# Optimization experiments

Measured on AMD Instinct MI355X. Metric: run time of the kernel, lower is better.

The kernel has to match this reference:

```python
import jax, jax.numpy as jnp
import numpy as np

N_EMBD = 2048
N_HEAD = 16
HEAD_DIM = N_EMBD // N_HEAD
LORA_R = 8
LORA_ALPHA = 1.0
LORA_SCALING = LORA_ALPHA / LORA_R


def setup_inputs() -> dict:
    key = jax.random.key(0)
    ks = jax.random.split(key, 10)
    B, T = 4, 2048
    init = LORA_ALPHA / LORA_R
    return {
        "x": jax.random.normal(ks[0], (B, T, N_EMBD), dtype=jnp.float32),
        "W_attn": jax.random.normal(ks[1], (N_EMBD, 3 * N_EMBD), dtype=jnp.float32) * 0.02,
        "b_attn": jnp.zeros((3 * N_EMBD,), dtype=jnp.float32),
        "lora_A_q": jax.random.normal(ks[2], (N_EMBD, LORA_R), dtype=jnp.float32) * init,
        "lora_B_q": jax.random.normal(ks[3], (LORA_R, N_EMBD), dtype=jnp.float32) * init,
        "lora_A_k": jax.random.normal(ks[4], (N_EMBD, LORA_R), dtype=jnp.float32) * init,
        "lora_B_k": jax.random.normal(ks[5], (LORA_R, N_EMBD), dtype=jnp.float32) * init,
        "W_proj": jax.random.normal(ks[6], (N_EMBD, N_EMBD), dtype=jnp.float32) * 0.02,
        "b_proj": jnp.zeros((N_EMBD,), dtype=jnp.float32),
    }


def _rotate_half(x):
    # torch: x1 = x[..., ::2]; x2 = x[..., 1::2]; cat((-x2, x1), -1)
    x1 = x[..., ::2]
    x2 = x[..., 1::2]
    return jnp.concatenate([-x2, x1], axis=-1)


def _rope_cos_sin(T, dtype):
    inv_freq = 1.0 / (10000.0 ** (jnp.arange(0, HEAD_DIM, 2, dtype=jnp.float32) / HEAD_DIM))
    t = jnp.arange(T, dtype=jnp.float32)
    freqs = jnp.einsum("i,j->ij", t, inv_freq)            # [T, D/2]
    emb = jnp.concatenate([freqs, freqs], axis=-1)          # [T, D]
    return jnp.cos(emb).astype(dtype), jnp.sin(emb).astype(dtype)


def reference(x, W_attn, b_attn, lora_A_q, lora_B_q, lora_A_k, lora_B_k, W_proj, b_proj):
    B, T, C = x.shape
    qkv = x @ W_attn + b_attn                                # [B,T,3C]
    q, k, v = jnp.split(qkv, 3, axis=2)
    # LoRA additions on q, k (applied to attn outputs, per module)
    q = q + (q @ lora_A_q) @ lora_B_q * LORA_SCALING
    k = k + (k @ lora_A_k) @ lora_B_k * LORA_SCALING

    def to_heads(z):
        return z.reshape(B, T, N_HEAD, HEAD_DIM).transpose(0, 2, 1, 3)  # [B,H,T,D]

    q, k, v = to_heads(q), to_heads(k), to_heads(v)
    cos, sin = _rope_cos_sin(T, x.dtype)                     # [T,D] each
    q = q * cos + _rotate_half(q) * sin
    k = k * cos + _rotate_half(k) * sin

    scale = 1.0 / jnp.sqrt(jnp.asarray(HEAD_DIM, dtype=x.dtype))
    scores = jnp.einsum("bhqd,bhkd->bhqk", q, k) * scale     # [B,H,T,T]
    causal = jnp.tril(jnp.ones((T, T), dtype=bool))
    scores = jnp.where(causal, scores, jnp.finfo(x.dtype).min)
    attn = jax.nn.softmax(scores, axis=-1)
    y = jnp.einsum("bhqk,bhkd->bhqd", attn, v)               # [B,H,T,D]
    y = y.transpose(0, 2, 1, 3).reshape(B, T, C)
    return y @ W_proj + b_proj
```

## Files before the change

kernel.cpp:

```cpp
#include <hip/hip_runtime.h>
#include <hip/hip_bf16.h>
#include <stdint.h>


typedef __attribute__((ext_vector_type(8))) short short8;
typedef __attribute__((ext_vector_type(4))) short short4v;
typedef __attribute__((ext_vector_type(4))) float floatx4;

#define EXP2F(x) __builtin_amdgcn_exp2f(x)

__device__ __forceinline__ float bf2f(short h) {
  union { unsigned int u; float f; } v;
  v.u = ((unsigned int)(unsigned short)h) << 16;
  return v.f;
}
__device__ __forceinline__ short f2bf(float f) {
  unsigned int u = __float_as_uint(f);
  unsigned int r = (u + 0x7FFFu + ((u >> 16) & 1u)) >> 16;
  return (short)r;
}
__device__ __forceinline__ short f2bf_n(float f) {
  __hip_bfloat16 h = __float2bfloat16(f);
  union { __hip_bfloat16 b; short s; } v; v.b = h; return v.s;
}

__device__ __forceinline__ void gload_lds16(const short* g, short* l) {
  __builtin_amdgcn_global_load_lds(
      (const __attribute__((address_space(1))) unsigned int*)g,
      (__attribute__((address_space(3))) unsigned int*)l, 16, 0, 0);
}

__device__ __forceinline__ void store_out(float* p, float v) { *p = v; }
__device__ __forceinline__ void store_out(short* p, float v) { *p = f2bf(v); }

__device__ __forceinline__ int xcd_swz(int orig, int nwg) {
  int q = nwg >> 3;
  return (orig & 7) * q + (orig >> 3);
}

#define SWZ(off, row) ((off) ^ (((row) & 7) << 3))

__global__ void k_f2b(const float* __restrict__ in, short* __restrict__ out, int n8) {
  int i = blockIdx.x * 256 + threadIdx.x;
  if (i >= n8) return;
  const float4* p = (const float4*)in + (size_t)i * 2;
  float4 a = p[0], b = p[1];
  short8 v;
  v[0] = f2bf(a.x); v[1] = f2bf(a.y); v[2] = f2bf(a.z); v[3] = f2bf(a.w);
  v[4] = f2bf(b.x); v[5] = f2bf(b.y); v[6] = f2bf(b.z); v[7] = f2bf(b.w);
  *(short8*)(out + (size_t)i * 8) = v;
}

__global__ void k_wT(const float* __restrict__ W, short* __restrict__ WT, int K, int N) {
  __shared__ float tile[32][33];
  int n0 = blockIdx.x * 32, k0 = blockIdx.y * 32;
  int tx = threadIdx.x, ty = threadIdx.y;
  #pragma unroll
  for (int i = 0; i < 4; i++)
    tile[ty + i * 8][tx] = W[(size_t)(k0 + ty + i * 8) * N + n0 + tx];
  __syncthreads();
  #pragma unroll
  for (int i = 0; i < 4; i++)
    WT[(size_t)(n0 + ty + i * 8) * K + k0 + tx] = f2bf(tile[tx][ty + i * 8]);
}

__global__ void k_ropetab(float* __restrict__ ct, float* __restrict__ st) {
  int t = blockIdx.x, j = threadIdx.x;
  float invf = powf(10000.0f, -(float)(2 * j) / 128.0f);
  float ang = (float)t * invf;
  ct[t * 64 + j] = cosf(ang);
  st[t * 64 + j] = sinf(ang);
}


#define GBAR __builtin_amdgcn_s_barrier();

#define RDA(QR) \
    _Pragma("unroll") for (int m_ = 0; m_ < 4; m_++) \
    _Pragma("unroll") for (int kk_ = 0; kk_ < 2; kk_++) { \
      int sA_ = ((QR) * 2 + wm) * 8192 + (m_ * 16 + c16) * 128 + kk_ * 64 + g * 16; \
      afr[m_][kk_] = *(const short8*)(Ab + ((sA_ ^ swzk) >> 1)); \
    }

#define RDBX(BB, QC, DST) \
    _Pragma("unroll") for (int n_ = 0; n_ < 2; n_++) \
    _Pragma("unroll") for (int kk_ = 0; kk_ < 2; kk_++) { \
      int sB_ = ((QC) * 4 + wn) * 4096 + (n_ * 16 + c16) * 128 + kk_ * 64 + g * 16; \
      DST[n_][kk_] = *(const short8*)((BB) + ((sB_ ^ swzk) >> 1)); \
    }

#define MM(QR, QC, BF) \
    __builtin_amdgcn_s_barrier(); \
    __builtin_amdgcn_s_setprio(1); \
    _Pragma("unroll") for (int kk_ = 0; kk_ < 2; kk_++) \
    _Pragma("unroll") for (int m_ = 0; m_ < 4; m_++) \
    _Pragma("unroll") for (int n_ = 0; n_ < 2; n_++) \
      acc[(QR) * 4 + m_][(QC) * 2 + n_] = __builtin_amdgcn_mfma_f32_16x16x32_bf16( \
          afr[m_][kk_], BF[n_][kk_], acc[(QR) * 4 + m_][(QC) * 2 + n_], 0, 0, 0); \
    __builtin_amdgcn_s_setprio(0);

template <typename OutT>
__global__ __launch_bounds__(512, 2) void k_gemm8(
    const short* __restrict__ A, const short* __restrict__ BT,
    const float* __restrict__ bias, OutT* __restrict__ C,
    int M, int N, int K)
{
  __shared__ __attribute__((aligned(16))) short lds[65536];
  const int tid = threadIdx.x;
  const int w = tid >> 6, l = tid & 63;
  const int g = l >> 4, c16 = l & 15;
  const int wm = w >> 2, wn = w & 3;
  const int swzk = (c16 & 7) << 4;

  const int nwg = gridDim.x * gridDim.y;
  const int wg = xcd_swz(blockIdx.y * gridDim.x + blockIdx.x, nwg);
  const int bm = wg % gridDim.x, bn = wg / gridDim.x;

  const short* Ablk = A + (size_t)bm * 256 * K;
  const short* Bblk = BT + (size_t)bn * 256 * K;

  floatx4 acc[8][4];
  #pragma unroll
  for (int i = 0; i < 8; i++)
    #pragma unroll
    for (int j = 0; j < 4; j++)
      acc[i][j] = (floatx4){0.f, 0.f, 0.f, 0.f};

  const int NT = K >> 6;
  const int L = NT >> 1;

  auto stageA = [&](int b, int h, int t) {
    short* dst = lds + b * 32768;
    int k0 = t * 64;
    #pragma unroll
    for (int j = 0; j < 2; j++) {
      int P = h * 2 + j;
      int sL = P * 8192 + tid * 16;
      int q = sL ^ (((sL >> 7) & 7) << 4);
      int row = (((((P & 1) << 1) | (P >> 1))) << 6) + ((sL >> 7) & 63);
      gload_lds16(Ablk + (size_t)row * K + k0 + ((q & 127) >> 1), dst + (sL >> 1));
    }
  };
  auto stageB = [&](int b, int h, int t) {
    short* dst = lds + b * 32768 + 16384;
    int k0 = t * 64;
    #pragma unroll
    for (int j = 0; j < 2; j++) {
      int sL = (h * 4 + 2 * j) * 4096 + tid * 16;
      int pos = sL >> 12;
      int q = sL ^ (((sL >> 7) & 7) << 4);
      int row = (((pos & 3) * 2 + (pos >> 2)) << 5) + ((sL >> 7) & 31);
      gload_lds16(Bblk + (size_t)row * K + k0 + ((q & 127) >> 1), dst + (sL >> 1));
    }
  };

  stageA(0, 0, 0); stageB(0, 0, 0); stageA(0, 1, 0); stageB(0, 1, 0);
  stageA(1, 0, 1); stageB(1, 0, 1); stageA(1, 1, 1); stageB(1, 1, 1);
  asm volatile("s_waitcnt vmcnt(8)" ::: "memory");
  __builtin_amdgcn_s_barrier();

  short8 bfr0[2][2], bfr1[2][2];
  RDBX(lds + 16384, 0, bfr0)

  #pragma unroll 1
  for (int i = 0; i < L; i++) {
    const int t2 = 2 * i + 2, t3 = 2 * i + 3;
    short8 afr[4][2];

    {
      const short* Ab = lds;
      RDA(0) if (i > 0) stageA(1, 1, 2 * i + 1);
      MM(0, 0, bfr0) GBAR
      RDBX(lds + 16384, 1, bfr1) if (t2 < NT) stageA(0, 0, t2);
      MM(0, 1, bfr1) GBAR
      RDA(1) if (t2 < NT) stageB(0, 0, t2);
      MM(1, 0, bfr0)
      if (t2 < NT) { asm volatile("s_waitcnt vmcnt(4)" ::: "memory"); }
      else         { asm volatile("s_waitcnt vmcnt(0)" ::: "memory"); }
      GBAR
      RDBX(lds + 49152, 0, bfr0) if (t2 < NT) stageB(0, 1, t2);
      MM(1, 1, bfr1) GBAR
    }
    {
      const short* Ab = lds + 32768;
      RDA(0) if (t2 < NT) stageA(0, 1, t2);
      MM(0, 0, bfr0) GBAR
      RDBX(lds + 49152, 1, bfr1) if (t3 < NT) stageA(1, 0, t3);
      MM(0, 1, bfr1) GBAR
      RDA(1) if (t3 < NT) stageB(1, 0, t3);
      MM(1, 0, bfr0)
      if (t3 < NT) { asm volatile("s_waitcnt vmcnt(4)" ::: "memory"); }
      else         { asm volatile("s_waitcnt vmcnt(0)" ::: "memory"); }
      GBAR
      if (t2 < NT) { RDBX(lds + 16384, 0, bfr0) }
      if (t3 < NT) stageB(1, 1, t3);
      MM(1, 1, bfr1) GBAR
    }
  }

  #pragma unroll
  for (int qr = 0; qr < 2; qr++)
    #pragma unroll
    for (int qc = 0; qc < 2; qc++)
      #pragma unroll
      for (int m = 0; m < 4; m++)
        #pragma unroll
        for (int n = 0; n < 2; n++) {
          int col = bn * 256 + wn * 64 + qc * 32 + n * 16 + c16;
          float bv = bias[col];
          #pragma unroll
          for (int r = 0; r < 4; r++) {
            size_t row = (size_t)bm * 256 + wm * 128 + qr * 64 + m * 16 + g * 4 + r;
            store_out(C + row * (size_t)N + col, acc[qr * 4 + m][qc * 2 + n][r] + bv);
          }
        }
}

__global__ __launch_bounds__(256, 2) void k_lorarope(
    short* __restrict__ qkv, const float* __restrict__ Aq, const float* __restrict__ Ak,
    const float* __restrict__ Bq, const float* __restrict__ Bk,
    const float* __restrict__ ct, const float* __restrict__ st)
{
  __shared__ float Bs[8 * 2048];
  __shared__ short Ls[2048];
  __shared__ float red[4][8];
  const int u = threadIdx.x;
  const int which = blockIdx.y;
  const float* Am = which ? Ak : Aq;
  const float* Bm = which ? Bk : Bq;
  const float qs = which ? 1.0f : 0.127517403f;

  #pragma unroll
  for (int i = 0; i < 16; i++) {
    int idx = (i * 256 + u) * 4;
    *(float4*)(Bs + idx) = *(const float4*)(Bm + idx);
  }
  float Areg[8][8];
  #pragma unroll
  for (int e = 0; e < 8; e++) {
    float4 a0 = *(const float4*)(Am + (size_t)(u * 8 + e) * 8);
    float4 a1 = *(const float4*)(Am + (size_t)(u * 8 + e) * 8 + 4);
    Areg[e][0] = a0.x; Areg[e][1] = a0.y; Areg[e][2] = a0.z; Areg[e][3] = a0.w;
    Areg[e][4] = a1.x; Areg[e][5] = a1.y; Areg[e][6] = a1.z; Areg[e][7] = a1.w;
  }
  __syncthreads();

  const int wv = u >> 6, l = u & 63;
  const int h = u >> 4, j0 = (u & 15) * 4;
  const int base = h * 128;
  const int t0 = blockIdx.x * 32;

  for (int tt = 0; tt < 32; tt++) {
    const int tok = t0 + tt;
    const int trow = tok & 2047;
    short* row = qkv + (size_t)tok * 6144 + which * 2048;

    __syncthreads();

    short8 q8 = *(const short8*)(row + u * 8);
    *(short8*)(Ls + u * 8) = q8;
    float part[8];
    #pragma unroll
    for (int r = 0; r < 8; r++) part[r] = 0.f;
    #pragma unroll
    for (int e = 0; e < 8; e++) {
      float qv = bf2f(q8[e]);
      #pragma unroll
      for (int r = 0; r < 8; r++) part[r] += qv * Areg[e][r];
    }
    #pragma unroll
    for (int r = 0; r < 8; r++)
      for (int off = 32; off > 0; off >>= 1)
        part[r] += __shfl_xor(part[r], off);
    if (l == 0) {
      #pragma unroll
      for (int r = 0; r < 8; r++) red[wv][r] = part[r];
    }
    __syncthreads();

    float Tr[8];
    #pragma unroll
    for (int r = 0; r < 8; r++)
      Tr[r] = (red[0][r] + red[1][r] + red[2][r] + red[3][r]) * 0.125f;

    float4 cv = *(const float4*)(ct + trow * 64 + j0);
    float4 sv = *(const float4*)(st + trow * 64 + j0);
    short4v qa4 = *(const short4v*)(Ls + base + j0);
    short4v qb4 = *(const short4v*)(Ls + base + 64 + j0);
    short8 qeo = *(const short8*)(Ls + base + 2 * j0);

    float o1[4], o2[4];
    #pragma unroll
    for (int j = 0; j < 4; j++) {
      float da = 0.f, db = 0.f, de = 0.f, dd = 0.f;
      #pragma unroll
      for (int r = 0; r < 8; r++) {
        const float* Br = Bs + r * 2048 + base;
        da += Tr[r] * Br[j0 + j];
        db += Tr[r] * Br[64 + j0 + j];
        de += Tr[r] * Br[2 * (j0 + j)];
        dd += Tr[r] * Br[2 * (j0 + j) + 1];
      }
      float qa = bf2f(qa4[j]) + da;
      float qb = bf2f(qb4[j]) + db;
      float qe = bf2f(qeo[2 * j]) + de;
      float qo = bf2f(qeo[2 * j + 1]) + dd;
      float c = ((const float*)&cv)[j], s = ((const float*)&sv)[j];
      o1[j] = (qa * c - qo * s) * qs;
      o2[j] = (qb * c + qe * s) * qs;
    }
    short4v w1, w2;
    #pragma unroll
    for (int j = 0; j < 4; j++) { w1[j] = f2bf(o1[j]); w2[j] = f2bf(o2[j]); }
    *(short4v*)(row + base + j0) = w1;
    *(short4v*)(row + base + 64 + j0) = w2;
  }
}

__global__ void k_vt(const short* __restrict__ qkv, short* __restrict__ vT) {
  __shared__ short tile[32][33];
  int bh = blockIdx.z, b = bh >> 4, h = bh & 15;
  int t0 = blockIdx.x * 32, d0 = blockIdx.y * 32;
  int tx = threadIdx.x, ty = threadIdx.y;
  #pragma unroll
  for (int i = 0; i < 4; i++) {
    int tt = t0 + ty + i * 8;
    tile[ty + i * 8][tx] = qkv[(size_t)(b * 2048 + tt) * 6144 + 4096 + h * 128 + d0 + tx];
  }
  __syncthreads();
  #pragma unroll
  for (int i = 0; i < 4; i++) {
    int d = d0 + ty + i * 8;
    vT[((size_t)bh * 128 + d) * 2048 + t0 + tx] = tile[tx][ty + i * 8];
  }
}

__global__ __launch_bounds__(256, 2) void k_attn(
    const short* __restrict__ qkv, const short* __restrict__ vT, short* __restrict__ y)
{
  __shared__ __attribute__((aligned(16))) short Ks[64 * 128];
  __shared__ __attribute__((aligned(16))) short Vs[128 * 64];
  __shared__ __attribute__((aligned(16))) short Ps[4 * 16 * 64];
  const int bh = blockIdx.x, b = bh >> 4, h = bh & 15;
  const int qt = 15 - (int)blockIdx.y;
  const int t = threadIdx.x, w = t >> 6, l = t & 63, g = l >> 4, c16 = l & 15;

  const int skr = t >> 2, sc0 = (t & 3) * 32;
  const int svd = t >> 1, sv0 = (t & 1) * 32;
  const short* kbase = qkv + (size_t)(b * 2048) * 6144 + 2048 + h * 128;
  const short* vbase = vT + (size_t)bh * 128 * 2048;
  short* Pw = Ps + w * (16 * 64);

  short8 onesv;
  #pragma unroll
  for (int e = 0; e < 8; e++) onesv[e] = (short)0x3F80;

  short8 qf[2][4];
  #pragma unroll
  for (int m = 0; m < 2; m++) {
    size_t goff = (size_t)(b * 2048 + qt * 128 + w * 32 + m * 16 + c16) * 6144 + h * 128;
    #pragma unroll
    for (int kf = 0; kf < 4; kf++)
      qf[m][kf] = *(const short8*)(qkv + goff + kf * 32 + 8 * g);
  }

  floatx4 o[2][8], ls[2];
  float mrow[2][4];
  #pragma unroll
  for (int m = 0; m < 2; m++) {
    #pragma unroll
    for (int nf = 0; nf < 8; nf++) o[m][nf] = (floatx4){0.f, 0.f, 0.f, 0.f};
    ls[m] = (floatx4){0.f, 0.f, 0.f, 0.f};
    #pragma unroll
    for (int r = 0; r < 4; r++) mrow[m][r] = -1e30f;
  }

  const int ntiles = 2 * qt + 2;

  short8 kreg[4], vreg[4];
  #pragma unroll
  for (int ii = 0; ii < 4; ii++) {
    kreg[ii] = *(const short8*)(kbase + (size_t)skr * 6144 + sc0 + ii * 8);
    vreg[ii] = *(const short8*)(vbase + (size_t)svd * 2048 + sv0 + ii * 8);
  }

  for (int kt = 0; kt < ntiles; kt++) {
    __syncthreads();
    #pragma unroll
    for (int ii = 0; ii < 4; ii++) {
      *(short8*)(Ks + SWZ(skr * 128 + sc0 + ii * 8, skr)) = kreg[ii];
      *(short8*)(Vs + SWZ(svd * 64 + sv0 + ii * 8, svd)) = vreg[ii];
    }
    __syncthreads();

    if (kt + 1 < ntiles) {
      #pragma unroll
      for (int ii = 0; ii < 4; ii++) {
        kreg[ii] = *(const short8*)(kbase + (size_t)((kt + 1) * 64 + skr) * 6144 + sc0 + ii * 8);
        vreg[ii] = *(const short8*)(vbase + (size_t)svd * 2048 + (kt + 1) * 64 + sv0 + ii * 8);
      }
    }

    floatx4 sc[2][4];
    #pragma unroll
    for (int m = 0; m < 2; m++)
      #pragma unroll
      for (int nf = 0; nf < 4; nf++) sc[m][nf] = (floatx4){0.f, 0.f, 0.f, 0.f};
    __builtin_amdgcn_s_setprio(1);
    #pragma unroll
    for (int kf = 0; kf < 4; kf++)
      #pragma unroll
      for (int nf = 0; nf < 4; nf++) {
        short8 kb = *(const short8*)(Ks + SWZ((nf * 16 + c16) * 128 + kf * 32 + 8 * g, c16));
        sc[0][nf] = __builtin_amdgcn_mfma_f32_16x16x32_bf16(qf[0][kf], kb, sc[0][nf], 0, 0, 0);
        sc[1][nf] = __builtin_amdgcn_mfma_f32_16x16x32_bf16(qf[1][kf], kb, sc[1][nf], 0, 0, 0);
      }
    __builtin_amdgcn_s_setprio(0);

    if (kt >= 2 * qt) {
      #pragma unroll
      for (int m = 0; m < 2; m++)
        #pragma unroll
        for (int nf = 0; nf < 4; nf++) {
          int key = kt * 64 + nf * 16 + c16;
          #pragma unroll
          for (int r = 0; r < 4; r++) {
            int qr = qt * 128 + w * 32 + m * 16 + g * 4 + r;
            if (key > qr) sc[m][nf][r] = -1e30f;
          }
        }
    }

    float need = -1e30f;
    #pragma unroll
    for (int m = 0; m < 2; m++)
      #pragma unroll
      for (int r = 0; r < 4; r++) {
        float rm = fmaxf(fmaxf(sc[m][0][r], sc[m][1][r]), fmaxf(sc[m][2][r], sc[m][3][r]));
        need = fmaxf(need, rm - mrow[m][r]);
      }
    if (!__all(need <= 11.0f)) {
      #pragma unroll
      for (int m = 0; m < 2; m++) {
        #pragma unroll
        for (int r = 0; r < 4; r++) {
          float rm = fmaxf(fmaxf(sc[m][0][r], sc[m][1][r]), fmaxf(sc[m][2][r], sc[m][3][r]));
          rm = fmaxf(rm, __shfl_xor(rm, 1));
          rm = fmaxf(rm, __shfl_xor(rm, 2));
          rm = fmaxf(rm, __shfl_xor(rm, 4));
          rm = fmaxf(rm, __shfl_xor(rm, 8));
          float mn = fmaxf(mrow[m][r], rm);
          float al = EXP2F(mrow[m][r] - mn);
          mrow[m][r] = mn;
          ls[m][r] *= al;
          #pragma unroll
          for (int nf = 0; nf < 8; nf++) o[m][nf][r] *= al;
        }
      }
    }

    short8 pa[2][2];
    #pragma unroll
    for (int m = 0; m < 2; m++) {
      #pragma unroll
      for (int r = 0; r < 4; r++) {
        int prow = g * 4 + r;
        #pragma unroll
        for (int nf = 0; nf < 4; nf++) {
          float p = EXP2F(sc[m][nf][r] - mrow[m][r]);
          Pw[SWZ(prow * 64 + nf * 16 + c16, prow)] = f2bf_n(p);
        }
      }
      #pragma unroll
      for (int kf = 0; kf < 2; kf++)
        pa[m][kf] = *(const short8*)(Pw + SWZ(c16 * 64 + kf * 32 + 8 * g, c16));
      if (m == 0) {
        asm volatile("s_waitcnt lgkmcnt(0)" ::: "memory");
        __builtin_amdgcn_sched_barrier(0);
      }
    }
    __builtin_amdgcn_s_setprio(1);
    #pragma unroll
    for (int m = 0; m < 2; m++)
      #pragma unroll
      for (int kf = 0; kf < 2; kf++)
        ls[m] = __builtin_amdgcn_mfma_f32_16x16x32_bf16(pa[m][kf], onesv, ls[m], 0, 0, 0);
    #pragma unroll
    for (int kf = 0; kf < 2; kf++)
      #pragma unroll
      for (int nf = 0; nf < 8; nf++) {
        short8 vb = *(const short8*)(Vs + SWZ((nf * 16 + c16) * 64 + kf * 32 + 8 * g, c16));
        o[0][nf] = __builtin_amdgcn_mfma_f32_16x16x32_bf16(pa[0][kf], vb, o[0][nf], 0, 0, 0);
        o[1][nf] = __builtin_amdgcn_mfma_f32_16x16x32_bf16(pa[1][kf], vb, o[1][nf], 0, 0, 0);
      }
    __builtin_amdgcn_s_setprio(0);
  }

  #pragma unroll
  for (int m = 0; m < 2; m++) {
    float ri[4];
    #pragma unroll
    for (int r = 0; r < 4; r++) ri[r] = 1.0f / ls[m][r];
    size_t yr0 = (size_t)(b * 2048 + qt * 128 + w * 32 + m * 16 + g * 4);
    #pragma unroll
    for (int nf = 0; nf < 8; nf++) {
      int col = h * 128 + nf * 16 + c16;
      #pragma unroll
      for (int r = 0; r < 4; r++)
        y[(yr0 + r) * 2048 + col] = f2bf_n(o[m][nf][r] * ri[r]);
    }
  }
}

extern "C" void kernel_launch(void* const* d_in, const int* in_sizes, int n_in,
                              void* d_out, int out_size, void* d_ws, size_t ws_size,
                              hipStream_t stream) {
  (void)in_sizes; (void)n_in; (void)out_size; (void)ws_size;
  const float* x      = (const float*)d_in[0];
  const float* W_attn = (const float*)d_in[1];
  const float* b_attn = (const float*)d_in[2];
  const float* Aq     = (const float*)d_in[3];
  const float* Bq     = (const float*)d_in[4];
  const float* Ak     = (const float*)d_in[5];
  const float* Bk     = (const float*)d_in[6];
  const float* W_proj = (const float*)d_in[7];
  const float* b_proj = (const float*)d_in[8];

  char* ws = (char*)d_ws;
  short* xb  = (short*)(ws + 0);
  short* WTa = (short*)(ws + 33554432);
  short* WTp = (short*)(ws + 58720256);
  short* qkv = (short*)(ws + 67108864);
  float* ct  = (float*)(ws + 168296448);
  float* st  = (float*)(ws + 168820736);
  short* vT  = (short*)(ws + 169345024);
  short* y   = xb;

  k_f2b<<<8192, 256, 0, stream>>>(x, xb, 2097152);
  k_wT<<<dim3(192, 64), dim3(32, 8), 0, stream>>>(W_attn, WTa, 2048, 6144);
  k_wT<<<dim3(64, 64), dim3(32, 8), 0, stream>>>(W_proj, WTp, 2048, 2048);
  k_ropetab<<<2048, 64, 0, stream>>>(ct, st);
  k_gemm8<short><<<dim3(32, 24), 512, 0, stream>>>(xb, WTa, b_attn, qkv, 8192, 6144, 2048);
  k_lorarope<<<dim3(256, 2), 256, 0, stream>>>(qkv, Aq, Ak, Bq, Bk, ct, st);
  k_vt<<<dim3(64, 4, 64), dim3(32, 8), 0, stream>>>(qkv, vT);
  k_attn<<<dim3(64, 16), 256, 0, stream>>>(qkv, vT, y);
  k_gemm8<float><<<dim3(32, 8), 512, 0, stream>>>(y, WTp, b_proj, (float*)d_out, 8192, 2048, 2048);
}
```

Baseline: 513.9 us.

## Fuse V transpose into QKV GEMM epilogue and peel pipelined GEMM loop

The QKV GEMM epilogue now writes the V columns straight into the transposed vT layout, so the separate k_vt transpose kernel and its extra global read and write of V are gone. The main K loop is also restructured: the first and last iterations are peeled out, which removes the per-step bounds checks, and finer-grained vmcnt waits are placed before each barrier. Together these aim to cut one kernel launch and its memory traffic and to tighten the load/compute overlap. The cost is that the vT stores are strided 8-byte writes, and correctness depends on the new waitcnt counts matching the number of outstanding loads.

```diff
diff --git a/kernel.cpp b/kernel.cpp
--- a/kernel.cpp
+++ b/kernel.cpp
@@ -74,6 +74,7 @@
 
 
 #define GBAR __builtin_amdgcn_s_barrier();
+#define VMW(N) asm volatile("s_waitcnt vmcnt(" #N ")" ::: "memory");
 
 #define RDA(QR) \
     _Pragma("unroll") for (int m_ = 0; m_ < 4; m_++) \
@@ -103,7 +104,7 @@
 __global__ __launch_bounds__(512, 2) void k_gemm8(
     const short* __restrict__ A, const short* __restrict__ BT,
     const float* __restrict__ bias, OutT* __restrict__ C,
-    int M, int N, int K)
+    int M, int N, int K, short* __restrict__ vTo)
 {
   __shared__ __attribute__((aligned(16))) short lds[65536];
   const int tid = threadIdx.x;
@@ -156,48 +157,90 @@
 
   stageA(0, 0, 0); stageB(0, 0, 0); stageA(0, 1, 0); stageB(0, 1, 0);
   stageA(1, 0, 1); stageB(1, 0, 1); stageA(1, 1, 1); stageB(1, 1, 1);
-  asm volatile("s_waitcnt vmcnt(8)" ::: "memory");
+  VMW(8)
   __builtin_amdgcn_s_barrier();
 
   short8 bfr0[2][2], bfr1[2][2];
   RDBX(lds + 16384, 0, bfr0)
 
+  {
+    short8 afr[4][2];
+    {
+      const short* Ab = lds;
+      RDA(0)                          MM(0, 0, bfr0) GBAR
+      RDBX(lds + 16384, 1, bfr1) stageA(0, 0, 2); MM(0, 1, bfr1) GBAR
+      RDA(1) stageB(0, 0, 2);         MM(1, 0, bfr0) VMW(4) GBAR
+      RDBX(lds + 49152, 0, bfr0) stageB(0, 1, 2); MM(1, 1, bfr1) GBAR
+    }
+    {
+      const short* Ab = lds + 32768;
+      RDA(0) stageA(0, 1, 2);         MM(0, 0, bfr0) GBAR
+      RDBX(lds + 49152, 1, bfr1) stageA(1, 0, 3); MM(0, 1, bfr1) GBAR
+      RDA(1) stageB(1, 0, 3);         MM(1, 0, bfr0) VMW(4) GBAR
+      RDBX(lds + 16384, 0, bfr0) stageB(1, 1, 3); MM(1, 1, bfr1) GBAR
+    }
+  }
+
   #pragma unroll 1
-  for (int i = 0; i < L; i++) {
+  for (int i = 1; i < L - 1; i++) {
     const int t2 = 2 * i + 2, t3 = 2 * i + 3;
     short8 afr[4][2];
-
     {
       const short* Ab = lds;
-      RDA(0) if (i > 0) stageA(1, 1, 2 * i + 1);
-      MM(0, 0, bfr0) GBAR
-      RDBX(lds + 16384, 1, bfr1) if (t2 < NT) stageA(0, 0, t2);
-      MM(0, 1, bfr1) GBAR
-      RDA(1) if (t2 < NT) stageB(0, 0, t2);
-      MM(1, 0, bfr0)
-      if (t2 < NT) { asm volatile("s_waitcnt vmcnt(4)" ::: "memory"); }
-      else         { asm volatile("s_waitcnt vmcnt(0)" ::: "memory"); }
-      GBAR
-      RDBX(lds + 49152, 0, bfr0) if (t2 < NT) stageB(0, 1, t2);
-      MM(1, 1, bfr1) GBAR
+      RDA(0) stageA(1, 1, 2 * i + 1); MM(0, 0, bfr0) VMW(10) GBAR
+      RDBX(lds + 16384, 1, bfr1) stageA(0, 0, t2); MM(0, 1, bfr1) VMW(10) GBAR
+      RDA(1) stageB(0, 0, t2);        MM(1, 0, bfr0) VMW(8)  GBAR
+      RDBX(lds + 49152, 0, bfr0) stageB(0, 1, t2); MM(1, 1, bfr1) VMW(12) GBAR
     }
     {
       const short* Ab = lds + 32768;
-      RDA(0) if (t2 < NT) stageA(0, 1, t2);
-      MM(0, 0, bfr0) GBAR
-      RDBX(lds + 49152, 1, bfr1) if (t3 < NT) stageA(1, 0, t3);
-      MM(0, 1, bfr1) GBAR
-      RDA(1) if (t3 < NT) stageB(1, 0, t3);
-      MM(1, 0, bfr0)
-      if (t3 < NT) { asm volatile("s_waitcnt vmcnt(4)" ::: "memory"); }
-      else         { asm volatile("s_waitcnt vmcnt(0)" ::: "memory"); }
-      GBAR
-      if (t2 < NT) { RDBX(lds + 16384, 0, bfr0) }
-      if (t3 < NT) stageB(1, 1, t3);
-      MM(1, 1, bfr1) GBAR
-    }
-  }
-
+      RDA(0) stageA(0, 1, t2);        MM(0, 0, bfr0) VMW(10) GBAR
+      RDBX(lds + 49152, 1, bfr1) stageA(1, 0, t3); MM(0, 1, bfr1) VMW(10) GBAR
+      RDA(1) stageB(1, 0, t3);        MM(1, 0, bfr0) VMW(8)  GBAR
+      RDBX(lds + 16384, 0, bfr0) stageB(1, 1, t3); MM(1, 1, bfr1) VMW(12) GBAR
+    }
+  }
+
+  {
+    short8 afr[4][2];
+    {
+      const short* Ab = lds;
+      RDA(0) stageA(1, 1, NT - 1);    MM(0, 0, bfr0) VMW(0) GBAR
+      RDBX(lds + 16384, 1, bfr1)      MM(0, 1, bfr1) GBAR
+      RDA(1)                          MM(1, 0, bfr0) GBAR
+      RDBX(lds + 49152, 0, bfr0)      MM(1, 1, bfr1) GBAR
+    }
+    {
+      const short* Ab = lds + 32768;
+      RDA(0)                          MM(0, 0, bfr0) GBAR
+      RDBX(lds + 49152, 1, bfr1)      MM(0, 1, bfr1) GBAR
+      RDA(1)                          MM(1, 0, bfr0) GBAR
+                                      MM(1, 1, bfr1)
+    }
+  }
+
+  if (vTo && bn >= 16) {
+    #pragma unroll
+    for (int qr = 0; qr < 2; qr++)
+      #pragma unroll
+      for (int qc = 0; qc < 2; qc++)
+        #pragma unroll
+        for (int m = 0; m < 4; m++)
+          #pragma unroll
+          for (int n = 0; n < 2; n++) {
+            int col = bn * 256 + wn * 64 + qc * 32 + n * 16 + c16;
+            float bv = bias[col];
+            int hh = (col - 4096) >> 7, dd = col & 127;
+            int rowb = bm * 256 + wm * 128 + qr * 64 + m * 16 + g * 4;
+            int bb = rowb >> 11, tt = rowb & 2047;
+            short4v pk;
+            #pragma unroll
+            for (int r = 0; r < 4; r++)
+              pk[r] = f2bf(acc[qr * 4 + m][qc * 2 + n][r] + bv);
+            *(short4v*)(vTo + ((size_t)((bb * 16 + hh) * 128 + dd)) * 2048 + tt) = pk;
+          }
+    return;
+  }
   #pragma unroll
   for (int qr = 0; qr < 2; qr++)
     #pragma unroll
@@ -314,24 +357,6 @@
     for (int j = 0; j < 4; j++) { w1[j] = f2bf(o1[j]); w2[j] = f2bf(o2[j]); }
     *(short4v*)(row + base + j0) = w1;
     *(short4v*)(row + base + 64 + j0) = w2;
-  }
-}
-
-__global__ void k_vt(const short* __restrict__ qkv, short* __restrict__ vT) {
-  __shared__ short tile[32][33];
-  int bh = blockIdx.z, b = bh >> 4, h = bh & 15;
-  int t0 = blockIdx.x * 32, d0 = blockIdx.y * 32;
-  int tx = threadIdx.x, ty = threadIdx.y;
-  #pragma unroll
-  for (int i = 0; i < 4; i++) {
-    int tt = t0 + ty + i * 8;
-    tile[ty + i * 8][tx] = qkv[(size_t)(b * 2048 + tt) * 6144 + 4096 + h * 128 + d0 + tx];
-  }
-  __syncthreads();
-  #pragma unroll
-  for (int i = 0; i < 4; i++) {
-    int d = d0 + ty + i * 8;
-    vT[((size_t)bh * 128 + d) * 2048 + t0 + tx] = tile[tx][ty + i * 8];
   }
 }
 
@@ -540,9 +565,8 @@
   k_wT<<<dim3(192, 64), dim3(32, 8), 0, stream>>>(W_attn, WTa, 2048, 6144);
   k_wT<<<dim3(64, 64), dim3(32, 8), 0, stream>>>(W_proj, WTp, 2048, 2048);
   k_ropetab<<<2048, 64, 0, stream>>>(ct, st);
-  k_gemm8<short><<<dim3(32, 24), 512, 0, stream>>>(xb, WTa, b_attn, qkv, 8192, 6144, 2048);
+  k_gemm8<short><<<dim3(32, 24), 512, 0, stream>>>(xb, WTa, b_attn, qkv, 8192, 6144, 2048, vT);
   k_lorarope<<<dim3(256, 2), 256, 0, stream>>>(qkv, Aq, Ak, Bq, Bk, ct, st);
-  k_vt<<<dim3(64, 4, 64), dim3(32, 8), 0, stream>>>(qkv, vT);
   k_attn<<<dim3(64, 16), 256, 0, stream>>>(qkv, vT, y);
-  k_gemm8<float><<<dim3(32, 8), 512, 0, stream>>>(y, WTp, b_proj, (float*)d_out, 8192, 2048, 2048);
-}
+  k_gemm8<float><<<dim3(32, 8), 512, 0, stream>>>(y, WTp, b_proj, (float*)d_out, 8192, 2048, 2048, nullptr);
+}
```

Result: slower. 722.3 us (+40.6%).

## Load K and V fragments directly from global memory in attention kernel

Applied to the files above, without the earlier changes.

Removes the shared-memory staging of K and V tiles, including the register prefetch and the two block-wide barriers per tile. Each wave now loads its MFMA operand fragments straight from global memory right before use. This cuts LDS traffic and synchronisation but drops the prefetch overlap, so every wave waits on global or cache latency inside the loop and the four waves re-read the same K/V data.

```diff
diff --git a/kernel.cpp b/kernel.cpp
--- a/kernel.cpp
+++ b/kernel.cpp
@@ -338,15 +338,11 @@
 __global__ __launch_bounds__(256, 2) void k_attn(
     const short* __restrict__ qkv, const short* __restrict__ vT, short* __restrict__ y)
 {
-  __shared__ __attribute__((aligned(16))) short Ks[64 * 128];
-  __shared__ __attribute__((aligned(16))) short Vs[128 * 64];
   __shared__ __attribute__((aligned(16))) short Ps[4 * 16 * 64];
   const int bh = blockIdx.x, b = bh >> 4, h = bh & 15;
   const int qt = 15 - (int)blockIdx.y;
   const int t = threadIdx.x, w = t >> 6, l = t & 63, g = l >> 4, c16 = l & 15;
 
-  const int skr = t >> 2, sc0 = (t & 3) * 32;
-  const int svd = t >> 1, sv0 = (t & 1) * 32;
   const short* kbase = qkv + (size_t)(b * 2048) * 6144 + 2048 + h * 128;
   const short* vbase = vT + (size_t)bh * 128 * 2048;
   short* Pw = Ps + w * (16 * 64);
@@ -377,45 +373,26 @@
 
   const int ntiles = 2 * qt + 2;
 
-  short8 kreg[4], vreg[4];
-  #pragma unroll
-  for (int ii = 0; ii < 4; ii++) {
-    kreg[ii] = *(const short8*)(kbase + (size_t)skr * 6144 + sc0 + ii * 8);
-    vreg[ii] = *(const short8*)(vbase + (size_t)svd * 2048 + sv0 + ii * 8);
-  }
-
   for (int kt = 0; kt < ntiles; kt++) {
-    __syncthreads();
-    #pragma unroll
-    for (int ii = 0; ii < 4; ii++) {
-      *(short8*)(Ks + SWZ(skr * 128 + sc0 + ii * 8, skr)) = kreg[ii];
-      *(short8*)(Vs + SWZ(svd * 64 + sv0 + ii * 8, svd)) = vreg[ii];
-    }
-    __syncthreads();
-
-    if (kt + 1 < ntiles) {
-      #pragma unroll
-      for (int ii = 0; ii < 4; ii++) {
-        kreg[ii] = *(const short8*)(kbase + (size_t)((kt + 1) * 64 + skr) * 6144 + sc0 + ii * 8);
-        vreg[ii] = *(const short8*)(vbase + (size_t)svd * 2048 + (kt + 1) * 64 + sv0 + ii * 8);
+    floatx4 sc[2][4];
+    #pragma unroll
+    for (int m = 0; m < 2; m++)
+      #pragma unroll
+      for (int nf = 0; nf < 4; nf++) sc[m][nf] = (floatx4){0.f, 0.f, 0.f, 0.f};
+    #pragma unroll
+    for (int nf = 0; nf < 4; nf++) {
+      const short* krow = kbase + (size_t)(kt * 64 + nf * 16 + c16) * 6144 + 8 * g;
+      short8 kb[4];
+      #pragma unroll
+      for (int kf = 0; kf < 4; kf++) kb[kf] = *(const short8*)(krow + kf * 32);
+      __builtin_amdgcn_s_setprio(1);
+      #pragma unroll
+      for (int kf = 0; kf < 4; kf++) {
+        sc[0][nf] = __builtin_amdgcn_mfma_f32_16x16x32_bf16(qf[0][kf], kb[kf], sc[0][nf], 0, 0, 0);
+        sc[1][nf] = __builtin_amdgcn_mfma_f32_16x16x32_bf16(qf[1][kf], kb[kf], sc[1][nf], 0, 0, 0);
       }
-    }
-
-    floatx4 sc[2][4];
-    #pragma unroll
-    for (int m = 0; m < 2; m++)
-      #pragma unroll
-      for (int nf = 0; nf < 4; nf++) sc[m][nf] = (floatx4){0.f, 0.f, 0.f, 0.f};
-    __builtin_amdgcn_s_setprio(1);
-    #pragma unroll
-    for (int kf = 0; kf < 4; kf++)
-      #pragma unroll
-      for (int nf = 0; nf < 4; nf++) {
-        short8 kb = *(const short8*)(Ks + SWZ((nf * 16 + c16) * 128 + kf * 32 + 8 * g, c16));
-        sc[0][nf] = __builtin_amdgcn_mfma_f32_16x16x32_bf16(qf[0][kf], kb, sc[0][nf], 0, 0, 0);
-        sc[1][nf] = __builtin_amdgcn_mfma_f32_16x16x32_bf16(qf[1][kf], kb, sc[1][nf], 0, 0, 0);
-      }
-    __builtin_amdgcn_s_setprio(0);
+      __builtin_amdgcn_s_setprio(0);
+    }
 
     if (kt >= 2 * qt) {
       #pragma unroll
@@ -479,21 +456,24 @@
         __builtin_amdgcn_sched_barrier(0);
       }
     }
-    __builtin_amdgcn_s_setprio(1);
+
     #pragma unroll
     for (int m = 0; m < 2; m++)
       #pragma unroll
       for (int kf = 0; kf < 2; kf++)
         ls[m] = __builtin_amdgcn_mfma_f32_16x16x32_bf16(pa[m][kf], onesv, ls[m], 0, 0, 0);
     #pragma unroll
-    for (int kf = 0; kf < 2; kf++)
-      #pragma unroll
-      for (int nf = 0; nf < 8; nf++) {
-        short8 vb = *(const short8*)(Vs + SWZ((nf * 16 + c16) * 64 + kf * 32 + 8 * g, c16));
-        o[0][nf] = __builtin_amdgcn_mfma_f32_16x16x32_bf16(pa[0][kf], vb, o[0][nf], 0, 0, 0);
-        o[1][nf] = __builtin_amdgcn_mfma_f32_16x16x32_bf16(pa[1][kf], vb, o[1][nf], 0, 0, 0);
-      }
-    __builtin_amdgcn_s_setprio(0);
+    for (int nf = 0; nf < 8; nf++) {
+      const short* vrow = vbase + (size_t)(nf * 16 + c16) * 2048 + kt * 64 + 8 * g;
+      short8 vb0 = *(const short8*)(vrow);
+      short8 vb1 = *(const short8*)(vrow + 32);
+      __builtin_amdgcn_s_setprio(1);
+      o[0][nf] = __builtin_amdgcn_mfma_f32_16x16x32_bf16(pa[0][0], vb0, o[0][nf], 0, 0, 0);
+      o[1][nf] = __builtin_amdgcn_mfma_f32_16x16x32_bf16(pa[1][0], vb0, o[1][nf], 0, 0, 0);
+      o[0][nf] = __builtin_amdgcn_mfma_f32_16x16x32_bf16(pa[0][1], vb1, o[0][nf], 0, 0, 0);
+      o[1][nf] = __builtin_amdgcn_mfma_f32_16x16x32_bf16(pa[1][1], vb1, o[1][nf], 0, 0, 0);
+      __builtin_amdgcn_s_setprio(0);
+    }
   }
 
   #pragma unroll
```

Result: slower. 652.1 us (+26.9%).
